# Performance work log

Hardware: AMD Instinct MI355X
Metric: run time of the kernel (lower is better)

The kernel has to match this reference:

```python
import jax, jax.numpy as jnp
import numpy as np

B, T, D, H, L, V = 2, 1024, 768, 12, 6, 32000
HD = D // H
EPS = 1e-5


def _ln(x, w, b):
    mu = jnp.mean(x, axis=-1, keepdims=True)
    var = jnp.mean((x - mu) ** 2, axis=-1, keepdims=True)
    return (x - mu) * jax.lax.rsqrt(var + EPS) * w + b


def setup_inputs() -> dict:
    key = jax.random.key(0)
    ks = jax.random.split(key, 20)
    s = 0.02
    inp = {
        "idx": jax.random.randint(ks[0], (B, T), 0, V),
        "wte": jax.random.normal(ks[1], (V, D), jnp.float32) * s,
        "wpe": jax.random.normal(ks[2], (T, D), jnp.float32) * s,
        # per-layer stacked params (leading dim L)
        "ln1_w": jnp.ones((L, D), jnp.float32),
        "ln1_b": jnp.zeros((L, D), jnp.float32),
        "attn_w": jax.random.normal(ks[3], (L, D, 3 * D), jnp.float32) * s,
        "attn_b": jnp.zeros((L, 3 * D), jnp.float32),
        "proj_w": jax.random.normal(ks[4], (L, D, D), jnp.float32) * s,
        "proj_b": jnp.zeros((L, D), jnp.float32),
        "ln2_w": jnp.ones((L, D), jnp.float32),
        "ln2_b": jnp.zeros((L, D), jnp.float32),
        "fc_w": jax.random.normal(ks[5], (L, D, 4 * D), jnp.float32) * s,
        "fc_b": jnp.zeros((L, 4 * D), jnp.float32),
        "fcproj_w": jax.random.normal(ks[6], (L, 4 * D, D), jnp.float32) * s,
        "fcproj_b": jnp.zeros((L, D), jnp.float32),
        "lnf_w": jnp.ones((D,), jnp.float32),
        "lnf_b": jnp.zeros((D,), jnp.float32),
        "head_w": jax.random.normal(ks[7], (D, V), jnp.float32) * s,
    }
    return inp


def _forward(idx, wte, wpe, ln1_w, ln1_b, attn_w, attn_b, proj_w, proj_b,
             ln2_w, ln2_b, fc_w, fc_b, fcproj_w, fcproj_b, lnf_w, lnf_b, head_w):
    t = idx.shape[1]
    x = wte[idx] + wpe[:t][None]  # [B,T,D]
    causal = jnp.tril(jnp.ones((t, t), bool))
    neg_inf = jnp.asarray(-jnp.inf, x.dtype)
    scale = 1.0 / np.sqrt(HD)

    def block(x, p):
        l1w, l1b, aw, ab, pw, pb, l2w, l2b, fw, fb, fpw, fpb = p
        h = _ln(x, l1w, l1b)
        qkv = h @ aw + ab  # [B,T,3D]
        q, k, v = jnp.split(qkv, 3, axis=-1)
        q = q.reshape(B, t, H, HD).transpose(0, 2, 1, 3)
        k = k.reshape(B, t, H, HD).transpose(0, 2, 1, 3)
        v = v.reshape(B, t, H, HD).transpose(0, 2, 1, 3)
        att = jnp.einsum('bhqd,bhkd->bhqk', q, k) * scale
        att = jnp.where(causal, att, neg_inf)
        att = jax.nn.softmax(att, axis=-1)
        y = jnp.einsum('bhqk,bhkd->bhqd', att, v)
        y = y.transpose(0, 2, 1, 3).reshape(B, t, D) @ pw + pb
        x = x + y
        h2 = _ln(x, l2w, l2b)
        m = jax.nn.gelu(h2 @ fw + fb, approximate=False) @ fpw + fpb
        return x + m, None

    layer_params = (ln1_w, ln1_b, attn_w, attn_b, proj_w, proj_b,
                    ln2_w, ln2_b, fc_w, fc_b, fcproj_w, fcproj_b)
    x, _ = jax.lax.scan(block, x, layer_params)
    logits = _ln(x, lnf_w, lnf_b) @ head_w  # [B,T,V]
    return logits


def reference(idx, wte, wpe, ln1_w, ln1_b, attn_w, attn_b, proj_w, proj_b,
              ln2_w, ln2_b, fc_w, fc_b, fcproj_w, fcproj_b, lnf_w, lnf_b, head_w):
    return _forward(idx, wte, wpe, ln1_w, ln1_b, attn_w, attn_b, proj_w, proj_b,
                    ln2_w, ln2_b, fc_w, fc_b, fcproj_w, fcproj_b, lnf_w, lnf_b, head_w)
```

## Files before the change

kernel.cpp:

```cpp
#include <hip/hip_runtime.h>
#include <hip/hip_bf16.h>
#include <math.h>

static constexpr int Bv = 2, Tv = 1024, Dv = 768, Hv = 12, Lv = 6, Vv = 32000, HDv = 64;
static constexpr int MROWS = Bv * Tv;

typedef __attribute__((ext_vector_type(8))) short bf16x8;
typedef __attribute__((ext_vector_type(8))) short short8;
typedef __attribute__((ext_vector_type(4))) short short4v;
typedef __attribute__((ext_vector_type(4))) float f32x4;

typedef __attribute__((address_space(1))) const void gvoid;
typedef __attribute__((address_space(3))) void svoid;
__device__ __forceinline__ void gld16(const void* g, void* s) {
  __builtin_amdgcn_global_load_lds((gvoid*)g, (svoid*)s, 16, 0, 0);
}
__device__ __forceinline__ short f2bf(float v) {
  __hip_bfloat16 hb = __float2bfloat16(v);
  return *reinterpret_cast<short*>(&hb);
}
__device__ __forceinline__ int xcd_remap(int lin, int nwg) {
  int q = nwg >> 3, r = nwg & 7;
  int xcd = lin & 7, idx = lin >> 3;
  return (xcd < r ? xcd * (q + 1) : r * (q + 1) + (xcd - r) * q) + idx;
}

__global__ __launch_bounds__(256) void embed_kernel(const int* __restrict__ idx,
                                                    const float* __restrict__ wte,
                                                    const float* __restrict__ wpe,
                                                    float* __restrict__ x) {
  int i4 = blockIdx.x * 256 + threadIdx.x;
  int total = MROWS * Dv / 4;
  if (i4 >= total) return;
  int d4 = (i4 % (Dv / 4)) * 4;
  int bt = i4 / (Dv / 4);
  int t  = bt % Tv;
  int id = idx[bt];
  float4 a = *(const float4*)(wte + (size_t)id * Dv + d4);
  float4 p = *(const float4*)(wpe + (size_t)t  * Dv + d4);
  a.x += p.x; a.y += p.y; a.z += p.z; a.w += p.w;
  *(float4*)(x + (size_t)bt * Dv + d4) = a;
}

__global__ __launch_bounds__(256) void ln_kernel(const float* __restrict__ x,
                                                 const float* __restrict__ w,
                                                 const float* __restrict__ b,
                                                 __hip_bfloat16* __restrict__ out) {
  int row = blockIdx.x;
  const float* xr = x + (size_t)row * Dv;
  int tid = threadIdx.x;
  float v0 = xr[tid], v1 = xr[tid + 256], v2 = xr[tid + 512];
  __shared__ float red[8];
  int wid = tid >> 6, lane = tid & 63;

  float s = v0 + v1 + v2;
  #pragma unroll
  for (int off = 1; off < 64; off <<= 1) s += __shfl_xor(s, off, 64);
  if (lane == 0) red[wid] = s;
  __syncthreads();
  s = red[0] + red[1] + red[2] + red[3];
  float mu = s * (1.0f / Dv);

  float d0 = v0 - mu, d1 = v1 - mu, d2 = v2 - mu;
  float q = d0 * d0 + d1 * d1 + d2 * d2;
  #pragma unroll
  for (int off = 1; off < 64; off <<= 1) q += __shfl_xor(q, off, 64);
  if (lane == 0) red[4 + wid] = q;
  __syncthreads();
  q = red[4] + red[5] + red[6] + red[7];
  float rs = rsqrtf(q * (1.0f / Dv) + 1e-5f);

  __hip_bfloat16* orow = out + (size_t)row * Dv;
  orow[tid]       = __float2bfloat16(d0 * rs * w[tid]       + b[tid]);
  orow[tid + 256] = __float2bfloat16(d1 * rs * w[tid + 256] + b[tid + 256]);
  orow[tid + 512] = __float2bfloat16(d2 * rs * w[tid + 512] + b[tid + 512]);
}

__device__ __forceinline__ void tcast_body(const float* __restrict__ W,
                                           __hip_bfloat16* __restrict__ Wt,
                                           int K, int N, int k0, int n0) {
  __shared__ float tile[32][33];
  int tx = threadIdx.x & 31, ty = threadIdx.x >> 5;
  #pragma unroll
  for (int r = 0; r < 32; r += 8)
    tile[ty + r][tx] = W[(size_t)(k0 + ty + r) * N + n0 + tx];
  __syncthreads();
  #pragma unroll
  for (int r = 0; r < 32; r += 8)
    Wt[(size_t)(n0 + ty + r) * K + k0 + tx] = __float2bfloat16(tile[tx][ty + r]);
}

__global__ __launch_bounds__(256) void tcast_kernel(const float* __restrict__ W,
                                                    __hip_bfloat16* __restrict__ Wt,
                                                    int K, int N) {
  tcast_body(W, Wt, K, N, blockIdx.y * 32, blockIdx.x * 32);
}

__global__ __launch_bounds__(256) void tcast4_kernel(const float* __restrict__ s0,
                                                     const float* __restrict__ s1,
                                                     const float* __restrict__ s2,
                                                     const float* __restrict__ s3,
                                                     __hip_bfloat16* __restrict__ d0,
                                                     __hip_bfloat16* __restrict__ d1,
                                                     __hip_bfloat16* __restrict__ d2,
                                                     __hip_bfloat16* __restrict__ d3) {
  int lin = blockIdx.x;
  const float* W; __hip_bfloat16* Wt; int K, N, loc;
  if (lin < 1728)      { W = s0; Wt = d0; K = 768;  N = 2304; loc = lin; }
  else if (lin < 2304) { W = s1; Wt = d1; K = 768;  N = 768;  loc = lin - 1728; }
  else if (lin < 4608) { W = s2; Wt = d2; K = 768;  N = 3072; loc = lin - 2304; }
  else                 { W = s3; Wt = d3; K = 3072; N = 768;  loc = lin - 4608; }
  int nb = N / 32;
  tcast_body(W, Wt, K, N, (loc / nb) * 32, (loc % nb) * 32);
}

template <bool GELU, bool OBF, bool VT>
__global__ __launch_bounds__(256) void gemm_kernel(const __hip_bfloat16* __restrict__ A,
                                                   const __hip_bfloat16* __restrict__ Wt,
                                                   const float* __restrict__ bias,
                                                   const float* __restrict__ resid,
                                                   void* __restrict__ outv,
                                                   __hip_bfloat16* __restrict__ vt,
                                                   int M, int N, int K) {
  __shared__ short As[128 * 32];
  __shared__ short Bs[128 * 32];
  int nwg = gridDim.x * gridDim.y;
  int wgid = xcd_remap(blockIdx.y * gridDim.x + blockIdx.x, nwg);
  int m0 = (wgid % gridDim.x) * 128, n0 = (wgid / gridDim.x) * 128;

  int tid = threadIdx.x;
  int w = tid >> 6, lane = tid & 63;
  int wr = w >> 1, wc = w & 1;

  f32x4 acc[4][4];
  #pragma unroll
  for (int m = 0; m < 4; ++m)
    #pragma unroll
    for (int n = 0; n < 4; ++n) acc[m][n] = (f32x4){0.f, 0.f, 0.f, 0.f};

  int lr = lane & 15, lk = lane >> 4;
  const short* abase = As + (wr * 64 + lr) * 32 + lk * 8;
  const short* bbase = Bs + (wc * 64 + lr) * 32 + lk * 8;
  int ko = (lane & 3) * 8;
  int rsub = lane >> 2;

  for (int k0 = 0; k0 < K; k0 += 32) {
    __syncthreads();
    #pragma unroll
    for (int e = 0; e < 2; ++e) {
      int chunk = e * 4 + w;
      int row = chunk * 16 + rsub;
      gld16(A  + (size_t)(m0 + row) * K + k0 + ko, As + chunk * 512);
      gld16(Wt + (size_t)(n0 + row) * K + k0 + ko, Bs + chunk * 512);
    }
    __syncthreads();
    bf16x8 af[4], bf[4];
    #pragma unroll
    for (int m = 0; m < 4; ++m) af[m] = *(const bf16x8*)(abase + m * 512);
    #pragma unroll
    for (int n = 0; n < 4; ++n) bf[n] = *(const bf16x8*)(bbase + n * 512);
    #pragma unroll
    for (int m = 0; m < 4; ++m)
      #pragma unroll
      for (int n = 0; n < 4; ++n)
        acc[m][n] = __builtin_amdgcn_mfma_f32_16x16x32_bf16(af[m], bf[n], acc[m][n], 0, 0, 0);
  }

  int row0 = m0 + wr * 64, col0 = n0 + wc * 64;
  float* outf = (float*)outv;
  __hip_bfloat16* outb = (__hip_bfloat16*)outv;
  #pragma unroll
  for (int n = 0; n < 4; ++n) {
    int col = col0 + n * 16 + lr;
    float bv = bias ? bias[col] : 0.f;
    #pragma unroll
    for (int m = 0; m < 4; ++m) {
      int rbase = row0 + m * 16 + lk * 4;
      float r4[4];
      #pragma unroll
      for (int j = 0; j < 4; ++j) {
        float v = acc[m][n][j] + bv;
        if (GELU) v = 0.5f * v * (1.0f + erff(v * 0.70710678118f));
        size_t o = (size_t)(rbase + j) * N + col;
        if (resid) v += resid[o];
        r4[j] = v;
        if (OBF) outb[o] = __float2bfloat16(v);
        else     outf[o] = v;
      }
      if (VT && col >= 2 * Dv) {
        int hh = (col - 2 * Dv) >> 6, dd = (col - 2 * Dv) & 63;
        int bb = rbase >> 10, t0 = rbase & 1023;
        short4v pk = {f2bf(r4[0]), f2bf(r4[1]), f2bf(r4[2]), f2bf(r4[3])};
        *(short4v*)(vt + (((size_t)(bb * Hv + hh) * HDv + dd) << 10) + t0) = pk;
      }
    }
  }
}

__global__ __launch_bounds__(256) void gemm64_kernel(const __hip_bfloat16* __restrict__ A,
                                                     const __hip_bfloat16* __restrict__ Wt,
                                                     const float* __restrict__ bias,
                                                     const float* __restrict__ resid,
                                                     float* __restrict__ out,
                                                     int M, int N, int K) {
  __shared__ short As[64 * 64];
  __shared__ short Bs[64 * 64];
  int nwg = gridDim.x * gridDim.y;
  int wgid = xcd_remap(blockIdx.y * gridDim.x + blockIdx.x, nwg);
  int m0 = (wgid % gridDim.x) * 64, n0 = (wgid / gridDim.x) * 64;

  int tid = threadIdx.x;
  int w = tid >> 6, lane = tid & 63;
  int wr = w >> 1, wc = w & 1;

  f32x4 acc[2][2];
  #pragma unroll
  for (int m = 0; m < 2; ++m)
    #pragma unroll
    for (int n = 0; n < 2; ++n) acc[m][n] = (f32x4){0.f, 0.f, 0.f, 0.f};

  int lr = lane & 15, lk = lane >> 4;
  int rsub = lane >> 3, go = lane & 7;

  for (int k0 = 0; k0 < K; k0 += 64) {
    __syncthreads();
    #pragma unroll
    for (int e = 0; e < 2; ++e) {
      int row = w * 16 + e * 8 + rsub;
      int gs = (go ^ rsub) * 8;
      gld16(A  + (size_t)(m0 + row) * K + k0 + gs, As + w * 1024 + e * 512);
      gld16(Wt + (size_t)(n0 + row) * K + k0 + gs, Bs + w * 1024 + e * 512);
    }
    __syncthreads();
    #pragma unroll
    for (int kf = 0; kf < 2; ++kf) {
      bf16x8 af[2], bf[2];
      #pragma unroll
      for (int m = 0; m < 2; ++m) {
        int row = wr * 32 + m * 16 + lr;
        af[m] = *(const bf16x8*)(As + row * 64 + (((kf * 4 + lk) ^ (row & 7)) * 8));
      }
      #pragma unroll
      for (int n = 0; n < 2; ++n) {
        int row = wc * 32 + n * 16 + lr;
        bf[n] = *(const bf16x8*)(Bs + row * 64 + (((kf * 4 + lk) ^ (row & 7)) * 8));
      }
      #pragma unroll
      for (int m = 0; m < 2; ++m)
        #pragma unroll
        for (int n = 0; n < 2; ++n)
          acc[m][n] = __builtin_amdgcn_mfma_f32_16x16x32_bf16(af[m], bf[n], acc[m][n], 0, 0, 0);
    }
  }

  int row0 = m0 + wr * 32, col0 = n0 + wc * 32;
  #pragma unroll
  for (int n = 0; n < 2; ++n) {
    int col = col0 + n * 16 + lr;
    float bv = bias ? bias[col] : 0.f;
    #pragma unroll
    for (int m = 0; m < 2; ++m) {
      int rbase = row0 + m * 16 + lk * 4;
      #pragma unroll
      for (int j = 0; j < 4; ++j) {
        float v = acc[m][n][j] + bv;
        size_t o = (size_t)(rbase + j) * N + col;
        if (resid) v += resid[o];
        out[o] = v;
      }
    }
  }
}

__global__ __launch_bounds__(512, 2) void gemm256_kernel(const __hip_bfloat16* __restrict__ A,
                                                         const __hip_bfloat16* __restrict__ Wt,
                                                         float* __restrict__ out,
                                                         int N, int K) {
  __shared__ short lds[65536];
  int nwg = gridDim.x * gridDim.y;
  int wgid = xcd_remap(blockIdx.y * gridDim.x + blockIdx.x, nwg);
  int m0 = (wgid % gridDim.x) * 256, n0 = (wgid / gridDim.x) * 256;

  int tid = threadIdx.x;
  int w = tid >> 6, lane = tid & 63;
  int wr = w >> 2, wc = w & 3;
  int lr = lane & 15, lk = lane >> 4;

  f32x4 acc[8][4];
  #pragma unroll
  for (int m = 0; m < 8; ++m)
    #pragma unroll
    for (int n = 0; n < 4; ++n) acc[m][n] = (f32x4){0.f, 0.f, 0.f, 0.f};

  int NT = K >> 6;

  auto stage = [&](int tau, int h) {
    int tsrc = tau < NT ? tau : NT - 1;
    const __hip_bfloat16* mat;
    size_t rb; int lofs;
    if (h == 0)      { mat = A;  rb = (size_t)m0;       lofs = 0; }
    else if (h == 1) { mat = Wt; rb = (size_t)n0;       lofs = 16384; }
    else if (h == 2) { mat = Wt; rb = (size_t)n0 + 128; lofs = 24576; }
    else             { mat = A;  rb = (size_t)m0 + 128; lofs = 8192; }
    short* lb = lds + (tau & 1) * 32768 + lofs;
    #pragma unroll
    for (int e = 0; e < 2; ++e) {
      int idx = e * 512 + tid;
      int r = idx >> 3, g = idx & 7;
      gld16(mat + (rb + r) * (size_t)K + tsrc * 64 + ((g ^ (r & 7)) * 8), lb + idx * 8);
    }
  };

  stage(0, 0); stage(0, 1); stage(0, 2); stage(0, 3);
  asm volatile("s_waitcnt vmcnt(4)" ::: "memory");
  asm volatile("s_barrier" ::: "memory");

  for (int tau = 0; tau < NT; ++tau) {
    const short* bufA = lds + (tau & 1) * 32768;
    const short* bufB = bufA + 16384;
    #pragma unroll
    for (int q = 0; q < 4; ++q) {
      stage(tau + 1, q);
      asm volatile("s_waitcnt vmcnt(4)" ::: "memory");
      int qm = q >> 1, qn = q & 1;
      const short* ab = bufA + qm * 8192;
      const short* bb = bufB + qn * 8192;
      bf16x8 af[4][2], bf[2][2];
      #pragma unroll
      for (int mi = 0; mi < 4; ++mi) {
        int ra = wr * 64 + mi * 16 + lr;
        #pragma unroll
        for (int kf = 0; kf < 2; ++kf)
          af[mi][kf] = *(const bf16x8*)(ab + ra * 64 + (((kf * 4 + lk) ^ (ra & 7)) * 8));
      }
      #pragma unroll
      for (int ni = 0; ni < 2; ++ni) {
        int rb2 = wc * 32 + ni * 16 + lr;
        #pragma unroll
        for (int kf = 0; kf < 2; ++kf)
          bf[ni][kf] = *(const bf16x8*)(bb + rb2 * 64 + (((kf * 4 + lk) ^ (rb2 & 7)) * 8));
      }
      asm volatile("s_barrier" ::: "memory");
      __builtin_amdgcn_s_setprio(1);
      #pragma unroll
      for (int mi = 0; mi < 4; ++mi)
        #pragma unroll
        for (int ni = 0; ni < 2; ++ni)
          #pragma unroll
          for (int kf = 0; kf < 2; ++kf)
            acc[qm * 4 + mi][qn * 2 + ni] = __builtin_amdgcn_mfma_f32_16x16x32_bf16(
                af[mi][kf], bf[ni][kf], acc[qm * 4 + mi][qn * 2 + ni], 0, 0, 0);
      __builtin_amdgcn_s_setprio(0);
      asm volatile("s_barrier" ::: "memory");
    }
  }

  #pragma unroll
  for (int gm = 0; gm < 8; ++gm) {
    int row = m0 + (gm >> 2) * 128 + wr * 64 + (gm & 3) * 16 + lk * 4;
    #pragma unroll
    for (int gn = 0; gn < 4; ++gn) {
      int col = n0 + (gn >> 1) * 128 + wc * 32 + (gn & 1) * 16 + lr;
      #pragma unroll
      for (int j = 0; j < 4; ++j)
        out[(size_t)(row + j) * N + col] = acc[gm][gn][j];
    }
  }
}

__global__ __launch_bounds__(256) void attn_kernel(const __hip_bfloat16* __restrict__ qkv,
                                                   const __hip_bfloat16* __restrict__ vt,
                                                   __hip_bfloat16* __restrict__ y) {
  __shared__ short Ks[64 * 64];
  __shared__ short Vts[64 * 64];
  __shared__ short Ps[4][16 * 64];
  int b = blockIdx.z, h = blockIdx.y;
  int qb = (gridDim.x - 1 - blockIdx.x) * 64;
  int tid = threadIdx.x;
  int w = tid >> 6, l = tid & 63;
  int lr = l & 15, lk = l >> 4;

  bf16x8 aq[2];
  {
    const __hip_bfloat16* qp = qkv + ((size_t)(b * Tv + qb + w * 16 + lr)) * 3 * Dv + h * HDv + lk * 8;
    aq[0] = *(const bf16x8*)qp;
    aq[1] = *(const bf16x8*)(qp + 32);
  }

  f32x4 o[4];
  #pragma unroll
  for (int n = 0; n < 4; ++n) o[n] = (f32x4){0.f, 0.f, 0.f, 0.f};
  float mrow[4] = {-1e30f, -1e30f, -1e30f, -1e30f};
  float lrow[4] = {0.f, 0.f, 0.f, 0.f};

  int r8 = l >> 3, c8 = l & 7;
  int nt = qb / 64 + 1;

  for (int kt = 0; kt < nt; ++kt) {
    int kbase = kt * 64;
    __syncthreads();
    #pragma unroll
    for (int e = 0; e < 2; ++e) {
      int r0 = w * 16 + e * 8;
      int rK = r0 + r8;
      int csK = c8 ^ (rK & 7);
      gld16(qkv + ((size_t)(b * Tv + kbase + rK)) * 3 * Dv + Dv + h * HDv + csK * 8,
            Ks + r0 * 64);
      gld16(vt + ((size_t)((b * Hv + h) * HDv + rK)) * Tv + kbase + csK * 8,
            Vts + r0 * 64);
    }
    __syncthreads();

    f32x4 s[4];
    #pragma unroll
    for (int n = 0; n < 4; ++n) s[n] = (f32x4){0.f, 0.f, 0.f, 0.f};
    #pragma unroll
    for (int kf = 0; kf < 2; ++kf)
      #pragma unroll
      for (int nf = 0; nf < 4; ++nf) {
        int row = nf * 16 + lr;
        int g = (kf * 4 + lk) ^ (row & 7);
        bf16x8 bk = *(const bf16x8*)(Ks + row * 64 + g * 8);
        s[nf] = __builtin_amdgcn_mfma_f32_16x16x32_bf16(aq[kf], bk, s[nf], 0, 0, 0);
      }
    #pragma unroll
    for (int nf = 0; nf < 4; ++nf)
      #pragma unroll
      for (int j = 0; j < 4; ++j) s[nf][j] *= 0.125f;

    if (kt == nt - 1) {
      #pragma unroll
      for (int nf = 0; nf < 4; ++nf) {
        int kl = nf * 16 + lr;
        #pragma unroll
        for (int j = 0; j < 4; ++j)
          if (kl > w * 16 + lk * 4 + j) s[nf][j] = -1e30f;
      }
    }

    float sc[4];
    #pragma unroll
    for (int j = 0; j < 4; ++j) {
      float pm = fmaxf(fmaxf(s[0][j], s[1][j]), fmaxf(s[2][j], s[3][j]));
      pm = fmaxf(pm, __shfl_xor(pm, 1, 64));
      pm = fmaxf(pm, __shfl_xor(pm, 2, 64));
      pm = fmaxf(pm, __shfl_xor(pm, 4, 64));
      pm = fmaxf(pm, __shfl_xor(pm, 8, 64));
      float mn = fmaxf(mrow[j], pm);
      sc[j] = __expf(mrow[j] - mn);
      mrow[j] = mn;
    }
    #pragma unroll
    for (int j = 0; j < 4; ++j) {
      float ls = 0.f;
      #pragma unroll
      for (int nf = 0; nf < 4; ++nf) {
        float p = __expf(s[nf][j] - mrow[j]);
        s[nf][j] = p;
        ls += p;
      }
      ls += __shfl_xor(ls, 1, 64);
      ls += __shfl_xor(ls, 2, 64);
      ls += __shfl_xor(ls, 4, 64);
      ls += __shfl_xor(ls, 8, 64);
      lrow[j] = lrow[j] * sc[j] + ls;
    }
    #pragma unroll
    for (int n = 0; n < 4; ++n)
      #pragma unroll
      for (int j = 0; j < 4; ++j) o[n][j] *= sc[j];

    short* pw = Ps[w];
    #pragma unroll
    for (int nf = 0; nf < 4; ++nf)
      #pragma unroll
      for (int j = 0; j < 4; ++j) {
        int ql = lk * 4 + j, k = nf * 16 + lr;
        pw[ql * 64 + (((k >> 3) ^ (ql & 7)) * 8) + (k & 7)] = f2bf(s[nf][j]);
      }
    bf16x8 pa[2];
    #pragma unroll
    for (int kf = 0; kf < 2; ++kf) {
      int g = (kf * 4 + lk) ^ (lr & 7);
      pa[kf] = *(const bf16x8*)(pw + lr * 64 + g * 8);
    }
    #pragma unroll
    for (int kf = 0; kf < 2; ++kf)
      #pragma unroll
      for (int nf = 0; nf < 4; ++nf) {
        int d = nf * 16 + lr;
        int g = (kf * 4 + lk) ^ (d & 7);
        bf16x8 bv = *(const bf16x8*)(Vts + d * 64 + g * 8);
        o[nf] = __builtin_amdgcn_mfma_f32_16x16x32_bf16(pa[kf], bv, o[nf], 0, 0, 0);
      }
  }

  #pragma unroll
  for (int j = 0; j < 4; ++j) lrow[j] = 1.f / lrow[j];
  #pragma unroll
  for (int nf = 0; nf < 4; ++nf)
    #pragma unroll
    for (int j = 0; j < 4; ++j) {
      size_t oidx = ((size_t)(b * Tv + qb + w * 16 + lk * 4 + j)) * Dv + h * HDv + nf * 16 + lr;
      y[oidx] = __float2bfloat16(o[nf][j] * lrow[j]);
    }
}

extern "C" void kernel_launch(void* const* d_in, const int* in_sizes, int n_in,
                              void* d_out, int out_size, void* d_ws, size_t ws_size,
                              hipStream_t stream) {
  const int*   idx      = (const int*)  d_in[0];
  const float* wte      = (const float*)d_in[1];
  const float* wpe      = (const float*)d_in[2];
  const float* ln1_w    = (const float*)d_in[3];
  const float* ln1_b    = (const float*)d_in[4];
  const float* attn_w   = (const float*)d_in[5];
  const float* attn_b   = (const float*)d_in[6];
  const float* proj_w   = (const float*)d_in[7];
  const float* proj_b   = (const float*)d_in[8];
  const float* ln2_w    = (const float*)d_in[9];
  const float* ln2_b    = (const float*)d_in[10];
  const float* fc_w     = (const float*)d_in[11];
  const float* fc_b     = (const float*)d_in[12];
  const float* fcproj_w = (const float*)d_in[13];
  const float* fcproj_b = (const float*)d_in[14];
  const float* lnf_w    = (const float*)d_in[15];
  const float* lnf_b    = (const float*)d_in[16];
  const float* head_w   = (const float*)d_in[17];
  float* outp = (float*)d_out;

  char* w8 = (char*)d_ws;
  float*          x    = (float*)w8;
  __hip_bfloat16* h    = (__hip_bfloat16*)(w8 + 6291456);
  __hip_bfloat16* qkv  = (__hip_bfloat16*)(w8 + 9437184);
  __hip_bfloat16* m4   = qkv;
  __hip_bfloat16* y    = (__hip_bfloat16*)(w8 + 22020096);
  __hip_bfloat16* vt   = (__hip_bfloat16*)(w8 + 25165824);
  __hip_bfloat16* wbuf = (__hip_bfloat16*)(w8 + 28311552);

  __hip_bfloat16* wb_attn   = wbuf;
  __hip_bfloat16* wb_proj   = wb_attn + (size_t)768 * 2304;
  __hip_bfloat16* wb_fc     = wb_proj + (size_t)768 * 768;
  __hip_bfloat16* wb_fcproj = wb_fc   + (size_t)768 * 3072;

  embed_kernel<<<(MROWS * Dv / 4 + 255) / 256, 256, 0, stream>>>(idx, wte, wpe, x);

  for (int l = 0; l < Lv; ++l) {
    ln_kernel<<<MROWS, 256, 0, stream>>>(x, ln1_w + (size_t)l * Dv, ln1_b + (size_t)l * Dv, h);

    tcast4_kernel<<<6912, 256, 0, stream>>>(
        attn_w   + (size_t)l * Dv * 3 * Dv,
        proj_w   + (size_t)l * Dv * Dv,
        fc_w     + (size_t)l * Dv * 4 * Dv,
        fcproj_w + (size_t)l * 4 * Dv * Dv,
        wb_attn, wb_proj, wb_fc, wb_fcproj);

    gemm_kernel<false, true, true><<<dim3(MROWS / 128, 3 * Dv / 128), 256, 0, stream>>>(
        h, wb_attn, attn_b + (size_t)l * 3 * Dv, nullptr, qkv, vt, MROWS, 3 * Dv, Dv);

    attn_kernel<<<dim3(Tv / 64, Hv, Bv), 256, 0, stream>>>(qkv, vt, y);

    gemm64_kernel<<<dim3(MROWS / 64, Dv / 64), 256, 0, stream>>>(
        y, wb_proj, proj_b + (size_t)l * Dv, x, x, MROWS, Dv, Dv);

    ln_kernel<<<MROWS, 256, 0, stream>>>(x, ln2_w + (size_t)l * Dv, ln2_b + (size_t)l * Dv, h);

    gemm_kernel<true, true, false><<<dim3(MROWS / 128, 4 * Dv / 128), 256, 0, stream>>>(
        h, wb_fc, fc_b + (size_t)l * 4 * Dv, nullptr, m4, nullptr, MROWS, 4 * Dv, Dv);

    gemm64_kernel<<<dim3(MROWS / 64, Dv / 64), 256, 0, stream>>>(
        m4, wb_fcproj, fcproj_b + (size_t)l * Dv, x, x, MROWS, Dv, 4 * Dv);
  }

  ln_kernel<<<MROWS, 256, 0, stream>>>(x, lnf_w, lnf_b, h);
  tcast_kernel<<<dim3(Vv / 32, Dv / 32), 256, 0, stream>>>(head_w, wbuf, Dv, Vv);
  gemm256_kernel<<<dim3(MROWS / 256, Vv / 256), 512, 0, stream>>>(
      h, wbuf, outp, Vv, Dv);
}
```

Before: 1.135 ms.

## Double-buffer LDS staging in GEMM and attention kernels, widen K-tile

The 128x128 GEMM moves to a 64-wide K tile with XOR-swizzled LDS layout and two LDS buffers, so the next tile's global-to-LDS load is issued while the current tile is multiplied. The 64x64 GEMM and the attention kernel get the same double-buffered K/V staging, and attention raises wave priority around its MFMA blocks. Each kernel also gets its own named wrapper per call site. The goal is to hide global-load latency behind MFMA work and cut one barrier per iteration, at the cost of twice the LDS per workgroup and possibly lower occupancy.

New measurement: 1.082 ms. -4.6%, faster.

```diff
diff --git a/kernel.cpp b/kernel.cpp
--- a/kernel.cpp
+++ b/kernel.cpp
@@ -115,15 +115,15 @@
 }
 
 template <bool GELU, bool OBF, bool VT>
-__global__ __launch_bounds__(256) void gemm_kernel(const __hip_bfloat16* __restrict__ A,
-                                                   const __hip_bfloat16* __restrict__ Wt,
-                                                   const float* __restrict__ bias,
-                                                   const float* __restrict__ resid,
-                                                   void* __restrict__ outv,
-                                                   __hip_bfloat16* __restrict__ vt,
-                                                   int M, int N, int K) {
-  __shared__ short As[128 * 32];
-  __shared__ short Bs[128 * 32];
+__device__ __forceinline__ void gemm128_body(const __hip_bfloat16* __restrict__ A,
+                                             const __hip_bfloat16* __restrict__ Wt,
+                                             const float* __restrict__ bias,
+                                             const float* __restrict__ resid,
+                                             void* __restrict__ outv,
+                                             __hip_bfloat16* __restrict__ vt,
+                                             int M, int N, int K) {
+  __shared__ short As[2][8192];
+  __shared__ short Bs[2][8192];
   int nwg = gridDim.x * gridDim.y;
   int wgid = xcd_remap(blockIdx.y * gridDim.x + blockIdx.x, nwg);
   int m0 = (wgid % gridDim.x) * 128, n0 = (wgid / gridDim.x) * 128;
@@ -131,6 +131,7 @@
   int tid = threadIdx.x;
   int w = tid >> 6, lane = tid & 63;
   int wr = w >> 1, wc = w & 1;
+  int lr = lane & 15, lk = lane >> 4;
 
   f32x4 acc[4][4];
   #pragma unroll
@@ -138,32 +139,46 @@
     #pragma unroll
     for (int n = 0; n < 4; ++n) acc[m][n] = (f32x4){0.f, 0.f, 0.f, 0.f};
 
-  int lr = lane & 15, lk = lane >> 4;
-  const short* abase = As + (wr * 64 + lr) * 32 + lk * 8;
-  const short* bbase = Bs + (wc * 64 + lr) * 32 + lk * 8;
-  int ko = (lane & 3) * 8;
-  int rsub = lane >> 2;
-
-  for (int k0 = 0; k0 < K; k0 += 32) {
+  auto stg = [&](int k0, int p) {
+    #pragma unroll
+    for (int e = 0; e < 4; ++e) {
+      int idx2 = e * 256 + tid;
+      int r = idx2 >> 3, g = idx2 & 7;
+      int gs = (g ^ (r & 7)) * 8;
+      gld16(A  + (size_t)(m0 + r) * K + k0 + gs, &As[p][idx2 * 8]);
+      gld16(Wt + (size_t)(n0 + r) * K + k0 + gs, &Bs[p][idx2 * 8]);
+    }
+  };
+
+  stg(0, 0);
+  __syncthreads();
+  int NK = K >> 6;
+  for (int kt = 0; kt < NK; ++kt) {
+    int p = kt & 1;
+    if (kt + 1 < NK) stg((kt + 1) << 6, p ^ 1);
+    bf16x8 af[4][2], bf[4][2];
+    #pragma unroll
+    for (int m = 0; m < 4; ++m) {
+      int ra = wr * 64 + m * 16 + lr;
+      #pragma unroll
+      for (int kf = 0; kf < 2; ++kf)
+        af[m][kf] = *(const bf16x8*)(&As[p][ra * 64 + (((kf * 4 + lk) ^ (ra & 7)) * 8)]);
+    }
+    #pragma unroll
+    for (int n = 0; n < 4; ++n) {
+      int rb = wc * 64 + n * 16 + lr;
+      #pragma unroll
+      for (int kf = 0; kf < 2; ++kf)
+        bf[n][kf] = *(const bf16x8*)(&Bs[p][rb * 64 + (((kf * 4 + lk) ^ (rb & 7)) * 8)]);
+    }
+    #pragma unroll
+    for (int kf = 0; kf < 2; ++kf)
+      #pragma unroll
+      for (int m = 0; m < 4; ++m)
+        #pragma unroll
+        for (int n = 0; n < 4; ++n)
+          acc[m][n] = __builtin_amdgcn_mfma_f32_16x16x32_bf16(af[m][kf], bf[n][kf], acc[m][n], 0, 0, 0);
     __syncthreads();
-    #pragma unroll
-    for (int e = 0; e < 2; ++e) {
-      int chunk = e * 4 + w;
-      int row = chunk * 16 + rsub;
-      gld16(A  + (size_t)(m0 + row) * K + k0 + ko, As + chunk * 512);
-      gld16(Wt + (size_t)(n0 + row) * K + k0 + ko, Bs + chunk * 512);
-    }
-    __syncthreads();
-    bf16x8 af[4], bf[4];
-    #pragma unroll
-    for (int m = 0; m < 4; ++m) af[m] = *(const bf16x8*)(abase + m * 512);
-    #pragma unroll
-    for (int n = 0; n < 4; ++n) bf[n] = *(const bf16x8*)(bbase + n * 512);
-    #pragma unroll
-    for (int m = 0; m < 4; ++m)
-      #pragma unroll
-      for (int n = 0; n < 4; ++n)
-        acc[m][n] = __builtin_amdgcn_mfma_f32_16x16x32_bf16(af[m], bf[n], acc[m][n], 0, 0, 0);
   }
 
   int row0 = m0 + wr * 64, col0 = n0 + wc * 64;
@@ -197,14 +212,28 @@
   }
 }
 
-__global__ __launch_bounds__(256) void gemm64_kernel(const __hip_bfloat16* __restrict__ A,
-                                                     const __hip_bfloat16* __restrict__ Wt,
-                                                     const float* __restrict__ bias,
-                                                     const float* __restrict__ resid,
-                                                     float* __restrict__ out,
-                                                     int M, int N, int K) {
-  __shared__ short As[64 * 64];
-  __shared__ short Bs[64 * 64];
+__global__ __launch_bounds__(256) void qkv_gemm_kernel(const __hip_bfloat16* A,
+                                                       const __hip_bfloat16* Wt,
+                                                       const float* bias,
+                                                       void* outv, __hip_bfloat16* vt,
+                                                       int M, int N, int K) {
+  gemm128_body<false, true, true>(A, Wt, bias, nullptr, outv, vt, M, N, K);
+}
+__global__ __launch_bounds__(256) void fc_gemm_kernel(const __hip_bfloat16* A,
+                                                      const __hip_bfloat16* Wt,
+                                                      const float* bias,
+                                                      void* outv, int M, int N, int K) {
+  gemm128_body<true, true, false>(A, Wt, bias, nullptr, outv, nullptr, M, N, K);
+}
+
+__device__ __forceinline__ void gemm64_body(const __hip_bfloat16* __restrict__ A,
+                                            const __hip_bfloat16* __restrict__ Wt,
+                                            const float* __restrict__ bias,
+                                            const float* __restrict__ resid,
+                                            float* __restrict__ out,
+                                            int M, int N, int K) {
+  __shared__ short As[2][4096];
+  __shared__ short Bs[2][4096];
   int nwg = gridDim.x * gridDim.y;
   int wgid = xcd_remap(blockIdx.y * gridDim.x + blockIdx.x, nwg);
   int m0 = (wgid % gridDim.x) * 64, n0 = (wgid / gridDim.x) * 64;
@@ -212,38 +241,43 @@
   int tid = threadIdx.x;
   int w = tid >> 6, lane = tid & 63;
   int wr = w >> 1, wc = w & 1;
-
-  f32x4 acc[2][2];
-  #pragma unroll
-  for (int m = 0; m < 2; ++m)
-    #pragma unroll
-    for (int n = 0; n < 2; ++n) acc[m][n] = (f32x4){0.f, 0.f, 0.f, 0.f};
-
   int lr = lane & 15, lk = lane >> 4;
   int rsub = lane >> 3, go = lane & 7;
 
-  for (int k0 = 0; k0 < K; k0 += 64) {
-    __syncthreads();
+  f32x4 acc[2][2];
+  #pragma unroll
+  for (int m = 0; m < 2; ++m)
+    #pragma unroll
+    for (int n = 0; n < 2; ++n) acc[m][n] = (f32x4){0.f, 0.f, 0.f, 0.f};
+
+  auto stg = [&](int k0, int p) {
     #pragma unroll
     for (int e = 0; e < 2; ++e) {
       int row = w * 16 + e * 8 + rsub;
       int gs = (go ^ rsub) * 8;
-      gld16(A  + (size_t)(m0 + row) * K + k0 + gs, As + w * 1024 + e * 512);
-      gld16(Wt + (size_t)(n0 + row) * K + k0 + gs, Bs + w * 1024 + e * 512);
-    }
-    __syncthreads();
+      gld16(A  + (size_t)(m0 + row) * K + k0 + gs, &As[p][w * 1024 + e * 512]);
+      gld16(Wt + (size_t)(n0 + row) * K + k0 + gs, &Bs[p][w * 1024 + e * 512]);
+    }
+  };
+
+  stg(0, 0);
+  __syncthreads();
+  int NK = K >> 6;
+  for (int kt = 0; kt < NK; ++kt) {
+    int p = kt & 1;
+    if (kt + 1 < NK) stg((kt + 1) << 6, p ^ 1);
     #pragma unroll
     for (int kf = 0; kf < 2; ++kf) {
       bf16x8 af[2], bf[2];
       #pragma unroll
       for (int m = 0; m < 2; ++m) {
         int row = wr * 32 + m * 16 + lr;
-        af[m] = *(const bf16x8*)(As + row * 64 + (((kf * 4 + lk) ^ (row & 7)) * 8));
+        af[m] = *(const bf16x8*)(&As[p][row * 64 + (((kf * 4 + lk) ^ (row & 7)) * 8)]);
       }
       #pragma unroll
       for (int n = 0; n < 2; ++n) {
         int row = wc * 32 + n * 16 + lr;
-        bf[n] = *(const bf16x8*)(Bs + row * 64 + (((kf * 4 + lk) ^ (row & 7)) * 8));
+        bf[n] = *(const bf16x8*)(&Bs[p][row * 64 + (((kf * 4 + lk) ^ (row & 7)) * 8)]);
       }
       #pragma unroll
       for (int m = 0; m < 2; ++m)
@@ -251,6 +285,7 @@
         for (int n = 0; n < 2; ++n)
           acc[m][n] = __builtin_amdgcn_mfma_f32_16x16x32_bf16(af[m], bf[n], acc[m][n], 0, 0, 0);
     }
+    __syncthreads();
   }
 
   int row0 = m0 + wr * 32, col0 = n0 + wc * 32;
@@ -270,6 +305,21 @@
       }
     }
   }
+}
+
+__global__ __launch_bounds__(256) void proj_gemm_kernel(const __hip_bfloat16* A,
+                                                        const __hip_bfloat16* Wt,
+                                                        const float* bias,
+                                                        const float* resid, float* out,
+                                                        int M, int N, int K) {
+  gemm64_body(A, Wt, bias, resid, out, M, N, K);
+}
+__global__ __launch_bounds__(256) void fcproj_gemm_kernel(const __hip_bfloat16* A,
+                                                          const __hip_bfloat16* Wt,
+                                                          const float* bias,
+                                                          const float* resid, float* out,
+                                                          int M, int N, int K) {
+  gemm64_body(A, Wt, bias, resid, out, M, N, K);
 }
 
 __global__ __launch_bounds__(512, 2) void gemm256_kernel(const __hip_bfloat16* __restrict__ A,
@@ -371,9 +421,9 @@
 __global__ __launch_bounds__(256) void attn_kernel(const __hip_bfloat16* __restrict__ qkv,
                                                    const __hip_bfloat16* __restrict__ vt,
                                                    __hip_bfloat16* __restrict__ y) {
-  __shared__ short Ks[64 * 64];
-  __shared__ short Vts[64 * 64];
-  __shared__ short Ps[4][16 * 64];
+  __shared__ short Ks[2][4096];
+  __shared__ short Vts[2][4096];
+  __shared__ short Ps[4][1024];
   int b = blockIdx.z, h = blockIdx.y;
   int qb = (gridDim.x - 1 - blockIdx.x) * 64;
   int tid = threadIdx.x;
@@ -396,33 +446,41 @@
   int r8 = l >> 3, c8 = l & 7;
   int nt = qb / 64 + 1;
 
-  for (int kt = 0; kt < nt; ++kt) {
-    int kbase = kt * 64;
-    __syncthreads();
+  auto stageKV = [&](int kt2, int p) {
+    int kbase = kt2 * 64;
     #pragma unroll
     for (int e = 0; e < 2; ++e) {
       int r0 = w * 16 + e * 8;
       int rK = r0 + r8;
       int csK = c8 ^ (rK & 7);
       gld16(qkv + ((size_t)(b * Tv + kbase + rK)) * 3 * Dv + Dv + h * HDv + csK * 8,
-            Ks + r0 * 64);
+            &Ks[p][r0 * 64]);
       gld16(vt + ((size_t)((b * Hv + h) * HDv + rK)) * Tv + kbase + csK * 8,
-            Vts + r0 * 64);
-    }
-    __syncthreads();
+            &Vts[p][r0 * 64]);
+    }
+  };
+
+  stageKV(0, 0);
+  __syncthreads();
+
+  for (int kt = 0; kt < nt; ++kt) {
+    int p = kt & 1;
+    if (kt + 1 < nt) stageKV(kt + 1, p ^ 1);
 
     f32x4 s[4];
     #pragma unroll
     for (int n = 0; n < 4; ++n) s[n] = (f32x4){0.f, 0.f, 0.f, 0.f};
+    __builtin_amdgcn_s_setprio(1);
     #pragma unroll
     for (int kf = 0; kf < 2; ++kf)
       #pragma unroll
       for (int nf = 0; nf < 4; ++nf) {
         int row = nf * 16 + lr;
         int g = (kf * 4 + lk) ^ (row & 7);
-        bf16x8 bk = *(const bf16x8*)(Ks + row * 64 + g * 8);
+        bf16x8 bk = *(const bf16x8*)(&Ks[p][row * 64 + g * 8]);
         s[nf] = __builtin_amdgcn_mfma_f32_16x16x32_bf16(aq[kf], bk, s[nf], 0, 0, 0);
       }
+    __builtin_amdgcn_s_setprio(0);
     #pragma unroll
     for (int nf = 0; nf < 4; ++nf)
       #pragma unroll
@@ -455,9 +513,9 @@
       float ls = 0.f;
       #pragma unroll
       for (int nf = 0; nf < 4; ++nf) {
-        float p = __expf(s[nf][j] - mrow[j]);
-        s[nf][j] = p;
-        ls += p;
+        float p2 = __expf(s[nf][j] - mrow[j]);
+        s[nf][j] = p2;
+        ls += p2;
       }
       ls += __shfl_xor(ls, 1, 64);
       ls += __shfl_xor(ls, 2, 64);
@@ -484,15 +542,18 @@
       int g = (kf * 4 + lk) ^ (lr & 7);
       pa[kf] = *(const bf16x8*)(pw + lr * 64 + g * 8);
     }
+    __builtin_amdgcn_s_setprio(1);
     #pragma unroll
     for (int kf = 0; kf < 2; ++kf)
       #pragma unroll
       for (int nf = 0; nf < 4; ++nf) {
         int d = nf * 16 + lr;
         int g = (kf * 4 + lk) ^ (d & 7);
-        bf16x8 bv = *(const bf16x8*)(Vts + d * 64 + g * 8);
+        bf16x8 bv = *(const bf16x8*)(&Vts[p][d * 64 + g * 8]);
         o[nf] = __builtin_amdgcn_mfma_f32_16x16x32_bf16(pa[kf], bv, o[nf], 0, 0, 0);
       }
+    __builtin_amdgcn_s_setprio(0);
+    __syncthreads();
   }
 
   #pragma unroll
@@ -555,20 +616,20 @@
         fcproj_w + (size_t)l * 4 * Dv * Dv,
         wb_attn, wb_proj, wb_fc, wb_fcproj);
 
-    gemm_kernel<false, true, true><<<dim3(MROWS / 128, 3 * Dv / 128), 256, 0, stream>>>(
-        h, wb_attn, attn_b + (size_t)l * 3 * Dv, nullptr, qkv, vt, MROWS, 3 * Dv, Dv);
+    qkv_gemm_kernel<<<dim3(MROWS / 128, 3 * Dv / 128), 256, 0, stream>>>(
+        h, wb_attn, attn_b + (size_t)l * 3 * Dv, qkv, vt, MROWS, 3 * Dv, Dv);
 
     attn_kernel<<<dim3(Tv / 64, Hv, Bv), 256, 0, stream>>>(qkv, vt, y);
 
-    gemm64_kernel<<<dim3(MROWS / 64, Dv / 64), 256, 0, stream>>>(
+    proj_gemm_kernel<<<dim3(MROWS / 64, Dv / 64), 256, 0, stream>>>(
         y, wb_proj, proj_b + (size_t)l * Dv, x, x, MROWS, Dv, Dv);
 
     ln_kernel<<<MROWS, 256, 0, stream>>>(x, ln2_w + (size_t)l * Dv, ln2_b + (size_t)l * Dv, h);
 
-    gemm_kernel<true, true, false><<<dim3(MROWS / 128, 4 * Dv / 128), 256, 0, stream>>>(
-        h, wb_fc, fc_b + (size_t)l * 4 * Dv, nullptr, m4, nullptr, MROWS, 4 * Dv, Dv);
-
-    gemm64_kernel<<<dim3(MROWS / 64, Dv / 64), 256, 0, stream>>>(
+    fc_gemm_kernel<<<dim3(MROWS / 128, 4 * Dv / 128), 256, 0, stream>>>(
+        h, wb_fc, fc_b + (size_t)l * 4 * Dv, m4, MROWS, 4 * Dv, Dv);
+
+    fcproj_gemm_kernel<<<dim3(MROWS / 64, Dv / 64), 256, 0, stream>>>(
         m4, wb_fcproj, fcproj_b + (size_t)l * Dv, x, x, MROWS, Dv, 4 * Dv);
   }
 
```
